# Optimization experiments

Hardware: AMD Instinct MI355X
Metric: run time of the kernel (lower is better)

## Reference

```python
import jax, jax.numpy as jnp
import numpy as np

K = 128      # knowledge_n (= net1 = prednet output width)
LOW = 64     # low_dim
PP = 64      # pp_dim
STU = 50000  # student_n
EXER = 20000 # exer_n
S_RANGES = [(0, 9999), (10000, 19999)]
NR = len(S_RANGES)
B = 4096


def setup_inputs() -> dict:
    key = jax.random.key(0)
    ks = jax.random.split(key, 16)

    def xavier(k, shape):
        fan_in, fan_out = shape[-1], shape[-2] if len(shape) > 1 else shape[-1]
        lim = np.sqrt(6.0 / (fan_in + fan_out))
        return jax.random.uniform(k, shape, jnp.float32, -lim, lim)

    return {
        "stu_id": jax.random.randint(ks[0], (B,), 0, STU),
        "exer_id": jax.random.randint(ks[1], (B,), 0, EXER),
        "kn_emb": jnp.ones((B, K), jnp.float32),
        "student_emb": xavier(ks[2], (NR, STU, LOW)),          # ParameterList stacked
        "prompt_stu": xavier(ks[3], (STU, PP)),
        "knowledge_emb": jax.random.normal(ks[4], (K, LOW), jnp.float32),
        "k_difficulty": xavier(ks[5], (EXER, LOW)),
        "s_exer_vectors": jax.random.uniform(ks[6], (NR, PP), jnp.float32),
        "W1": xavier(ks[7], (K, K + LOW)),                      # prednet_full1 (no bias)
        "W2": xavier(ks[8], (K, K + LOW)),                      # prednet_full2 (no bias)
        "W3": xavier(ks[9], (1, K)),                            # prednet_full3
        "b3": jnp.zeros((1,), jnp.float32),
        "fc1_W": xavier(ks[10], (K, PP + K)),
        "fc1_b": jnp.zeros((K,), jnp.float32),
        "fc2_W": xavier(ks[11], (K, PP + K)),
        "fc2_b": jnp.zeros((K,), jnp.float32),
    }


def reference(stu_id, exer_id, kn_emb, student_emb, prompt_stu, knowledge_emb,
              k_difficulty, s_exer_vectors, W1, W2, W3, b3, fc1_W, fc1_b, fc2_W, fc2_b):
    sig = jax.nn.sigmoid
    kle = knowledge_emb  # [K, LOW]

    # --- student side ---
    # prompt_stu.repeat(NR, 1) then index_select == index prompt_stu with stu_id % STU
    p_stu = prompt_stu[stu_id % STU]                              # [B, PP]
    stu_cat = student_emb.reshape(NR * STU, LOW)                  # concat of ParameterList
    old_stu = sig(stu_cat[stu_id] @ kle.T)                        # [B, K]
    stu_e = sig(jnp.concatenate([p_stu, old_stu], 1) @ fc1_W.T + fc1_b)  # [B, K]

    # --- exercise side ---
    counts = np.array([r[1] - r[0] + 1 for r in S_RANGES])
    temp_vectors = jnp.repeat(s_exer_vectors, counts, axis=0, total_repeat_length=EXER)
    p_exer = sig(temp_vectors[exer_id])                           # [B, PP]
    old_exer = sig(sig(k_difficulty[exer_id]) @ kle.T)            # [B, K]
    exer_e = sig(jnp.concatenate([p_exer, old_exer], 1) @ fc2_W.T + fc2_b)  # [B, K]

    # --- per-concept interaction ---
    # cat([x_broadcast, kn_vector], 2) @ W.T splits into x @ Wa.T + kle @ Wb.T
    W1a, W1b = W1[:, :K], W1[:, K:]
    W2a, W2b = W2[:, :K], W2[:, K:]
    preference = sig((stu_e @ W1a.T)[:, None, :] + (kle @ W1b.T)[None, :, :])   # [B, K, K]
    diff = sig((exer_e @ W2a.T)[:, None, :] + (kle @ W2b.T)[None, :, :])        # [B, K, K]

    o = sig((preference - diff) @ W3.T + b3)                      # [B, K, 1]
    sum_out = jnp.sum(o * kn_emb[:, :, None], axis=1)             # [B, 1]
    count = jnp.sum(kn_emb, axis=1, keepdims=True)
    return sum_out / count
```

## Files before the change

### kernel.cpp

```cpp
#include <hip/hip_runtime.h>
#include <hip/hip_bf16.h>

#define STUN   50000
#define BATCH  4096
#define LOG2E  1.4426950408889634f

__device__ __forceinline__ float fexp2(float x){ return __builtin_amdgcn_exp2f(x); }
__device__ __forceinline__ float frcp (float x){ return __builtin_amdgcn_rcpf(x); }
__device__ __forceinline__ float fsig (float x){ return frcp(1.0f + fexp2(-LOG2E * x)); }

__global__ __launch_bounds__(128) void k_pre(
    const float* __restrict__ kle,
    const float* __restrict__ W1,
    const float* __restrict__ W2,
    const float* __restrict__ fc1_W,
    const float* __restrict__ fc2_W,
    float* __restrict__ kleT,
    float* __restrict__ fc1T,
    float* __restrict__ fc2T,
    float* __restrict__ W1aT,
    float* __restrict__ W2aT,
    float* __restrict__ E1i,
    float* __restrict__ E2i)
{
    const int bid = blockIdx.x;
    const int t   = threadIdx.x;
    if (bid < 64) {
        const int u = bid;
        kleT[u * 128 + t] = kle[t * 64 + u];
    } else if (bid < 256) {
        const int u = bid - 64;
        fc1T[u * 128 + t] = fc1_W[t * 192 + u];
    } else if (bid < 448) {
        const int u = bid - 256;
        fc2T[u * 128 + t] = fc2_W[t * 192 + u];
    } else if (bid < 576) {
        const int u = bid - 448;
        W1aT[u * 128 + t] = W1[t * 192 + u];
    } else if (bid < 704) {
        const int u = bid - 576;
        W2aT[u * 128 + t] = W2[t * 192 + u];
    } else if (bid < 832) {
        const int j = bid - 704;
        float acc = 0.f;
        #pragma unroll
        for (int u4 = 0; u4 < 16; ++u4) {
            const float4 kv = *(const float4*)&kle[t * 64 + u4 * 4];
            const float4 wv = *(const float4*)&W1[j * 192 + 128 + u4 * 4];
            acc += kv.x * wv.x + kv.y * wv.y + kv.z * wv.z + kv.w * wv.w;
        }
        E1i[((j >> 2) * 128 + t) * 4 + (j & 3)] = fexp2(-LOG2E * acc);
    } else {
        const int j = bid - 832;
        float acc = 0.f;
        #pragma unroll
        for (int u4 = 0; u4 < 16; ++u4) {
            const float4 kv = *(const float4*)&kle[t * 64 + u4 * 4];
            const float4 wv = *(const float4*)&W2[j * 192 + 128 + u4 * 4];
            acc += kv.x * wv.x + kv.y * wv.y + kv.z * wv.z + kv.w * wv.w;
        }
        E2i[((j >> 2) * 128 + t) * 4 + (j & 3)] = fexp2(-LOG2E * acc);
    }
}

__global__ __launch_bounds__(512, 4) void k_fused(
    const int*   __restrict__ stu_id,
    const int*   __restrict__ exer_id,
    const float* __restrict__ student_emb,
    const float* __restrict__ prompt_stu,
    const float* __restrict__ k_diff,
    const float* __restrict__ s_exer,
    const float* __restrict__ kleT,
    const float* __restrict__ fc1T,
    const float* __restrict__ fc2T,
    const float* __restrict__ W1aT,
    const float* __restrict__ W2aT,
    const float* __restrict__ fc1_b,
    const float* __restrict__ fc2_b,
    const float* __restrict__ E1i,
    const float* __restrict__ E2i,
    const float* __restrict__ W3,
    const float* __restrict__ b3,
    const float* __restrict__ kn,
    float* __restrict__ out)
{
    __shared__ __align__(16) float sh_in [4][64][8];
    __shared__ __align__(16) float sh_old[2][128][12];
    __shared__ __align__(16) float sh_e  [2][128][12];
    __shared__ __align__(16) float ses   [2][8][128];
    __shared__ __align__(16) float red   [4][8][128];
    __shared__ float red2_o[8][2];
    __shared__ float red2_k[8][2];

    const int t  = threadIdx.x;
    const int b0 = blockIdx.x * 8;

    {
        const int g   = t >> 6;
        const int u   = t & 63;
        const int sid = stu_id[b0 + g];
        const int eid = exer_id[b0 + g];
        const int er  = (eid >= 10000) ? 1 : 0;
        sh_in[0][u][g] = student_emb[sid * 64 + u];
        sh_in[1][u][g] = fsig(k_diff[eid * 64 + u]);
        sh_in[2][u][g] = prompt_stu[(sid % STUN) * 64 + u];
        sh_in[3][u][g] = fsig(s_exer[er * 64 + u]);
    }
    __syncthreads();

    const int w    = t >> 6;
    const int half = w & 1;
    const int iqo  = w >> 1;
    const int l    = t & 63;
    const int ul   = l >> 4;
    const int bs   = (l >> 3) & 1;
    const int iql  = l & 7;
    const int iq   = iqo * 8 + iql;
    const int bq   = bs * 4;

    float a[4][4];

#define CLR { _Pragma("unroll") for (int c = 0; c < 4; ++c) \
              _Pragma("unroll") for (int b = 0; b < 4; ++b) a[c][b] = 0.f; }

#define FMAC(c, wc) { \
    a[c][0] = fmaf(wc, x0.x, a[c][0]); a[c][1] = fmaf(wc, x0.y, a[c][1]); \
    a[c][2] = fmaf(wc, x0.z, a[c][2]); a[c][3] = fmaf(wc, x0.w, a[c][3]); }

#define GSTEP(wp, xp) { \
    const float4 w4 = *(const float4*)(wp); \
    const float4 x0 = *(const float4*)(xp); \
    FMAC(0, w4.x); FMAC(1, w4.y); FMAC(2, w4.z); FMAC(3, w4.w); }

#define COMBINE { _Pragma("unroll") for (int c = 0; c < 4; ++c) \
    _Pragma("unroll") for (int b = 0; b < 4; ++b) { \
        float v = a[c][b]; \
        v += __shfl_xor(v, 16); \
        v += __shfl_xor(v, 32); \
        a[c][b] = v; } }

    CLR;
    #pragma unroll 4
    for (int u = ul; u < 64; u += 4)
        GSTEP(&kleT[u * 128 + iq * 4], &sh_in[half][u][bq]);
    COMBINE;
    if (ul == 0) {
        #pragma unroll
        for (int c = 0; c < 4; ++c)
            *(float4*)&sh_old[half][iq * 4 + c][bq] =
                make_float4(fsig(a[c][0]), fsig(a[c][1]), fsig(a[c][2]), fsig(a[c][3]));
    }
    __syncthreads();

    CLR;
    {
        const float* fcT = half ? fc2T : fc1T;
        #pragma unroll 4
        for (int u = ul; u < 64; u += 4)
            GSTEP(&fcT[u * 128 + iq * 4], &sh_in[2 + half][u][bq]);
        #pragma unroll 4
        for (int u = 64 + ul; u < 192; u += 4)
            GSTEP(&fcT[u * 128 + iq * 4], &sh_old[half][u - 64][bq]);
    }
    COMBINE;
    if (ul == 0) {
        const float* fcb = half ? fc2_b : fc1_b;
        #pragma unroll
        for (int c = 0; c < 4; ++c) {
            const float bias = fcb[iq * 4 + c];
            *(float4*)&sh_e[half][iq * 4 + c][bq] =
                make_float4(fsig(a[c][0] + bias), fsig(a[c][1] + bias),
                            fsig(a[c][2] + bias), fsig(a[c][3] + bias));
        }
    }
    __syncthreads();

    CLR;
    {
        const float* WT = half ? W2aT : W1aT;
        #pragma unroll 4
        for (int u = ul; u < 128; u += 4)
            GSTEP(&WT[u * 128 + iq * 4], &sh_e[half][u][bq]);
    }
    COMBINE;
    if (ul == 0) {
        #pragma unroll
        for (int c = 0; c < 4; ++c) {
            #pragma unroll
            for (int b = 0; b < 4; ++b)
                ses[half][bq + b][iq * 4 + c] = fexp2(-LOG2E * a[c][b]);
        }
    }
#undef CLR
#undef FMAC
#undef GSTEP
#undef COMBINE
    __syncthreads();

    const int k  = t & 127;
    const int jq = t >> 7;

    const float4* E1v = (const float4*)E1i + k;
    const float4* E2v = (const float4*)E2i + k;

    float acc[8];
    #pragma unroll
    for (int b = 0; b < 8; ++b) acc[b] = 0.f;

#define COMP(acc_, s1c, s2c, e1c, e2c, w3c) { \
        const float uu = (s1c) * (e1c); \
        const float vv = (s2c) * (e2c); \
        const float dd = frcp((1.f + uu) * (1.f + vv)); \
        acc_ = fmaf((vv - uu) * dd, (w3c), acc_); }

    #pragma unroll 2
    for (int i = 0; i < 8; ++i) {
        const int j4 = jq * 8 + i;
        const int j  = j4 * 4;
        const float4 e1 = E1v[j4 * 128];
        const float4 e2 = E2v[j4 * 128];
        const float4 w3 = *(const float4*)&W3[j];
        #pragma unroll
        for (int b = 0; b < 8; ++b) {
            const float4 p1 = *(const float4*)&ses[0][b][j];
            const float4 p2 = *(const float4*)&ses[1][b][j];
            COMP(acc[b], p1.x, p2.x, e1.x, e2.x, w3.x);
            COMP(acc[b], p1.y, p2.y, e1.y, e2.y, w3.y);
            COMP(acc[b], p1.z, p2.z, e1.z, e2.z, w3.z);
            COMP(acc[b], p1.w, p2.w, e1.w, e2.w, w3.w);
        }
    }
#undef COMP

    #pragma unroll
    for (int b = 0; b < 8; ++b) red[jq][b][k] = acc[b];
    __syncthreads();

    {
        const float bb3 = b3[0];
        float co[2], ck[2];
        #pragma unroll
        for (int h = 0; h < 2; ++h) {
            const int item = t + h * 512;
            const int b    = item >> 7;
            const int kk   = item & 127;
            const float s  = red[0][b][kk] + red[1][b][kk]
                           + red[2][b][kk] + red[3][b][kk];
            const float o  = fsig(s + bb3);
            const float kv = kn[(b0 + b) * 128 + kk];
            co[h] = o * kv;
            ck[h] = kv;
        }
        #pragma unroll
        for (int off = 1; off < 64; off <<= 1) {
            co[0] += __shfl_xor(co[0], off);
            ck[0] += __shfl_xor(ck[0], off);
            co[1] += __shfl_xor(co[1], off);
            ck[1] += __shfl_xor(ck[1], off);
        }
        if ((t & 63) == 0) {
            const int b_  = w >> 1;
            const int kh  = w & 1;
            red2_o[b_][kh]     = co[0];
            red2_k[b_][kh]     = ck[0];
            red2_o[b_ + 4][kh] = co[1];
            red2_k[b_ + 4][kh] = ck[1];
        }
    }
    __syncthreads();
    if (t < 8) {
        const float so = red2_o[t][0] + red2_o[t][1];
        const float sk = red2_k[t][0] + red2_k[t][1];
        out[b0 + t] = so / sk;
    }
}

extern "C" void kernel_launch(void* const* d_in, const int* in_sizes, int n_in,
                              void* d_out, int out_size, void* d_ws, size_t ws_size,
                              hipStream_t stream)
{
    const int*   stu_id      = (const int*)  d_in[0];
    const int*   exer_id     = (const int*)  d_in[1];
    const float* kn_emb      = (const float*)d_in[2];
    const float* student_emb = (const float*)d_in[3];
    const float* prompt_stu  = (const float*)d_in[4];
    const float* kle         = (const float*)d_in[5];
    const float* k_diff      = (const float*)d_in[6];
    const float* s_exer      = (const float*)d_in[7];
    const float* W1          = (const float*)d_in[8];
    const float* W2          = (const float*)d_in[9];
    const float* W3          = (const float*)d_in[10];
    const float* b3          = (const float*)d_in[11];
    const float* fc1_W       = (const float*)d_in[12];
    const float* fc1_b       = (const float*)d_in[13];
    const float* fc2_W       = (const float*)d_in[14];
    const float* fc2_b       = (const float*)d_in[15];
    float* out = (float*)d_out;

    float* ws   = (float*)d_ws;
    float* kleT = ws;
    float* fc1T = kleT + 8192;
    float* fc2T = fc1T + 24576;
    float* W1aT = fc2T + 24576;
    float* W2aT = W1aT + 16384;
    float* E1i  = W2aT + 16384;
    float* E2i  = E1i  + 16384;

    k_pre  <<<960, 128, 0, stream>>>(kle, W1, W2, fc1_W, fc2_W,
                                     kleT, fc1T, fc2T, W1aT, W2aT, E1i, E2i);
    k_fused<<<BATCH / 8, 512, 0, stream>>>(stu_id, exer_id, student_emb, prompt_stu,
                                           k_diff, s_exer, kleT, fc1T, fc2T,
                                           W1aT, W2aT, fc1_b, fc2_b,
                                           E1i, E2i, W3, b3, kn_emb, out);
}
```

Measured before the change: 47.42 us.

## Halve fused block to 4 batch rows with 256 threads and swizzled shared layout

```diff
diff --git a/kernel.cpp b/kernel.cpp
--- a/kernel.cpp
+++ b/kernel.cpp
@@ -8,6 +8,8 @@
 __device__ __forceinline__ float fexp2(float x){ return __builtin_amdgcn_exp2f(x); }
 __device__ __forceinline__ float frcp (float x){ return __builtin_amdgcn_rcpf(x); }
 __device__ __forceinline__ float fsig (float x){ return frcp(1.0f + fexp2(-LOG2E * x)); }
+
+#define SWZ(idx) ((idx) * 8 + ((((idx) >> 2) & 7) << 2))
 
 __global__ __launch_bounds__(128) void k_pre(
     const float* __restrict__ kle,
@@ -63,7 +65,7 @@
     }
 }
 
-__global__ __launch_bounds__(512, 4) void k_fused(
+__global__ __launch_bounds__(256, 6) void k_fused(
     const int*   __restrict__ stu_id,
     const int*   __restrict__ exer_id,
     const float* __restrict__ student_emb,
@@ -84,16 +86,16 @@
     const float* __restrict__ kn,
     float* __restrict__ out)
 {
-    __shared__ __align__(16) float sh_in [4][64][8];
-    __shared__ __align__(16) float sh_old[2][128][12];
-    __shared__ __align__(16) float sh_e  [2][128][12];
-    __shared__ __align__(16) float ses   [2][8][128];
-    __shared__ __align__(16) float red   [4][8][128];
-    __shared__ float red2_o[8][2];
-    __shared__ float red2_k[8][2];
+    __shared__ __align__(16) float sh_in[4][64][4];
+    __shared__ __align__(16) float s_old[2][1056];
+    __shared__ __align__(16) float s_e  [2][1056];
+    __shared__ __align__(16) float ses  [2][4][128];
+    __shared__ __align__(16) float red  [2][4][128];
+    __shared__ float red2_o[4][2];
+    __shared__ float red2_k[4][2];
 
     const int t  = threadIdx.x;
-    const int b0 = blockIdx.x * 8;
+    const int b0 = blockIdx.x * 4;
 
     {
         const int g   = t >> 6;
@@ -109,14 +111,11 @@
     __syncthreads();
 
     const int w    = t >> 6;
-    const int half = w & 1;
-    const int iqo  = w >> 1;
     const int l    = t & 63;
     const int ul   = l >> 4;
-    const int bs   = (l >> 3) & 1;
+    const int half = (l >> 3) & 1;
     const int iql  = l & 7;
-    const int iq   = iqo * 8 + iql;
-    const int bq   = bs * 4;
+    const int iq   = w * 8 + iql;
 
     float a[4][4];
 
@@ -141,13 +140,15 @@
 
     CLR;
     #pragma unroll 4
-    for (int u = ul; u < 64; u += 4)
-        GSTEP(&kleT[u * 128 + iq * 4], &sh_in[half][u][bq]);
+    for (int s = 0; s < 16; ++s) {
+        const int u = ul + s * 4;
+        GSTEP(&kleT[u * 128 + iq * 4], &sh_in[half][u][0]);
+    }
     COMBINE;
     if (ul == 0) {
         #pragma unroll
         for (int c = 0; c < 4; ++c)
-            *(float4*)&sh_old[half][iq * 4 + c][bq] =
+            *(float4*)&s_old[half][SWZ(iq * 4 + c)] =
                 make_float4(fsig(a[c][0]), fsig(a[c][1]), fsig(a[c][2]), fsig(a[c][3]));
     }
     __syncthreads();
@@ -156,11 +157,15 @@
     {
         const float* fcT = half ? fc2T : fc1T;
         #pragma unroll 4
-        for (int u = ul; u < 64; u += 4)
-            GSTEP(&fcT[u * 128 + iq * 4], &sh_in[2 + half][u][bq]);
+        for (int s = 0; s < 16; ++s) {
+            const int u = ul + s * 4;
+            GSTEP(&fcT[u * 128 + iq * 4], &sh_in[2 + half][u][0]);
+        }
         #pragma unroll 4
-        for (int u = 64 + ul; u < 192; u += 4)
-            GSTEP(&fcT[u * 128 + iq * 4], &sh_old[half][u - 64][bq]);
+        for (int s = 0; s < 32; ++s) {
+            const int u = ul + s * 4;
+            GSTEP(&fcT[(64 + u) * 128 + iq * 4], &s_old[half][SWZ(u)]);
+        }
     }
     COMBINE;
     if (ul == 0) {
@@ -168,7 +173,7 @@
         #pragma unroll
         for (int c = 0; c < 4; ++c) {
             const float bias = fcb[iq * 4 + c];
-            *(float4*)&sh_e[half][iq * 4 + c][bq] =
+            *(float4*)&s_e[half][SWZ(iq * 4 + c)] =
                 make_float4(fsig(a[c][0] + bias), fsig(a[c][1] + bias),
                             fsig(a[c][2] + bias), fsig(a[c][3] + bias));
         }
@@ -179,8 +184,10 @@
     {
         const float* WT = half ? W2aT : W1aT;
         #pragma unroll 4
-        for (int u = ul; u < 128; u += 4)
-            GSTEP(&WT[u * 128 + iq * 4], &sh_e[half][u][bq]);
+        for (int s = 0; s < 32; ++s) {
+            const int u = ul + s * 4;
+            GSTEP(&WT[u * 128 + iq * 4], &s_e[half][SWZ(u)]);
+        }
     }
     COMBINE;
     if (ul == 0) {
@@ -188,7 +195,7 @@
         for (int c = 0; c < 4; ++c) {
             #pragma unroll
             for (int b = 0; b < 4; ++b)
-                ses[half][bq + b][iq * 4 + c] = fexp2(-LOG2E * a[c][b]);
+                ses[half][b][iq * 4 + c] = fexp2(-LOG2E * a[c][b]);
         }
     }
 #undef CLR
@@ -203,9 +210,9 @@
     const float4* E1v = (const float4*)E1i + k;
     const float4* E2v = (const float4*)E2i + k;
 
-    float acc[8];
+    float acc[4];
     #pragma unroll
-    for (int b = 0; b < 8; ++b) acc[b] = 0.f;
+    for (int b = 0; b < 4; ++b) acc[b] = 0.f;
 
 #define COMP(acc_, s1c, s2c, e1c, e2c, w3c) { \
         const float uu = (s1c) * (e1c); \
@@ -214,14 +221,14 @@
         acc_ = fmaf((vv - uu) * dd, (w3c), acc_); }
 
     #pragma unroll 2
-    for (int i = 0; i < 8; ++i) {
-        const int j4 = jq * 8 + i;
+    for (int i = 0; i < 16; ++i) {
+        const int j4 = jq * 16 + i;
         const int j  = j4 * 4;
         const float4 e1 = E1v[j4 * 128];
         const float4 e2 = E2v[j4 * 128];
         const float4 w3 = *(const float4*)&W3[j];
         #pragma unroll
-        for (int b = 0; b < 8; ++b) {
+        for (int b = 0; b < 4; ++b) {
             const float4 p1 = *(const float4*)&ses[0][b][j];
             const float4 p2 = *(const float4*)&ses[1][b][j];
             COMP(acc[b], p1.x, p2.x, e1.x, e2.x, w3.x);
@@ -233,7 +240,7 @@
 #undef COMP
 
     #pragma unroll
-    for (int b = 0; b < 8; ++b) red[jq][b][k] = acc[b];
+    for (int b = 0; b < 4; ++b) red[jq][b][k] = acc[b];
     __syncthreads();
 
     {
@@ -241,11 +248,9 @@
         float co[2], ck[2];
         #pragma unroll
         for (int h = 0; h < 2; ++h) {
-            const int item = t + h * 512;
-            const int b    = item >> 7;
-            const int kk   = item & 127;
-            const float s  = red[0][b][kk] + red[1][b][kk]
-                           + red[2][b][kk] + red[3][b][kk];
+            const int b  = (t >> 7) + 2 * h;
+            const int kk = t & 127;
+            const float s  = red[0][b][kk] + red[1][b][kk];
             const float o  = fsig(s + bb3);
             const float kv = kn[(b0 + b) * 128 + kk];
             co[h] = o * kv;
@@ -259,16 +264,16 @@
             ck[1] += __shfl_xor(ck[1], off);
         }
         if ((t & 63) == 0) {
-            const int b_  = w >> 1;
-            const int kh  = w & 1;
-            red2_o[b_][kh]     = co[0];
-            red2_k[b_][kh]     = ck[0];
-            red2_o[b_ + 4][kh] = co[1];
-            red2_k[b_ + 4][kh] = ck[1];
-        }
-    }
-    __syncthreads();
-    if (t < 8) {
+            const int kh = w & 1;
+            const int bb = w >> 1;
+            red2_o[bb][kh]     = co[0];
+            red2_k[bb][kh]     = ck[0];
+            red2_o[bb + 2][kh] = co[1];
+            red2_k[bb + 2][kh] = ck[1];
+        }
+    }
+    __syncthreads();
+    if (t < 4) {
         const float so = red2_o[t][0] + red2_o[t][1];
         const float sk = red2_k[t][0] + red2_k[t][1];
         out[b0 + t] = so / sk;
@@ -308,7 +313,7 @@
 
     k_pre  <<<960, 128, 0, stream>>>(kle, W1, W2, fc1_W, fc2_W,
                                      kleT, fc1T, fc2T, W1aT, W2aT, E1i, E2i);
-    k_fused<<<BATCH / 8, 512, 0, stream>>>(stu_id, exer_id, student_emb, prompt_stu,
+    k_fused<<<BATCH / 4, 256, 0, stream>>>(stu_id, exer_id, student_emb, prompt_stu,
                                            k_diff, s_exer, kleT, fc1T, fc2T,
                                            W1aT, W2aT, fc1_b, fc2_b,
                                            E1i, E2i, W3, b3, kn_emb, out);
```

Result: slower. 49.31 us (+4.0%).
